# Kernel tuning notes

Hardware: AMD Instinct MI355X
Metric: run time of the kernel (lower is better)

The kernel has to match this reference:

```python
import jax, jax.numpy as jnp
import numpy as np

N = 50000   # nodes
E = 800000  # edges
C = 64      # channels per head (= n_channel)
H = 2       # heads
EPS = 1e-5


def _layernorm(x, g, b):
    m = jnp.mean(x, axis=-1, keepdims=True)
    v = jnp.mean((x - m) ** 2, axis=-1, keepdims=True)
    return (x - m) / jnp.sqrt(v + EPS) * g + b


def setup_inputs() -> dict:
    key = jax.random.key(0)
    ks = jax.random.split(key, 20)
    r = lambda k, shape: (jax.random.normal(k, shape, jnp.float32) * 0.05)
    inp = {
        "x": jax.random.normal(ks[0], (N, C), jnp.float32),
        "edge_index": jax.random.randint(ks[1], (2, E), 0, N, jnp.int64),
        "edge_attr": jax.random.normal(ks[2], (E, 1), jnp.float32),
        # TransformerConv params (PyG): lin_query/key/value: in=C -> H*C with bias
        "Wq": r(ks[3], (H * C, C)), "bq": r(ks[4], (H * C,)),
        "Wk": r(ks[5], (H * C, C)), "bk": r(ks[6], (H * C,)),
        "Wv": r(ks[7], (H * C, C)), "bv": r(ks[8], (H * C,)),
        # lin_edge: edge_dim=1 -> H*C, no bias
        "We": r(ks[9], (H * C, 1)),
        # lin_skip (root weight, concat=False -> out=C), with bias
        "Wskip": r(ks[10], (C, C)), "bskip": r(ks[11], (C,)),
        # shell linear + layernorms
        "Wl": r(ks[12], (C, C)), "bl": r(ks[13], (C,)),
        "g0": jnp.ones((C,), jnp.float32), "b0": jnp.zeros((C,), jnp.float32),
        "g1": jnp.ones((C,), jnp.float32), "b1": jnp.zeros((C,), jnp.float32),
    }
    return inp


def _transformer_conv(x, src, dst, edge_attr, Wq, bq, Wk, bk, Wv, bv, We, Wskip, bskip):
    q = (x @ Wq.T + bq).reshape(N, H, C)
    k = (x @ Wk.T + bk).reshape(N, H, C)
    v = (x @ Wv.T + bv).reshape(N, H, C)
    e = (edge_attr @ We.T).reshape(E, H, C)        # [E,H,C]
    k_j = k[src] + e                               # gather + edge key
    v_j = v[src] + e
    alpha = jnp.einsum('ehc,ehc->eh', q[dst], k_j) / jnp.sqrt(jnp.float32(C))
    # segment softmax over destination nodes
    amax = jax.ops.segment_max(alpha, dst, num_segments=N)      # [N,H]
    ex = jnp.exp(alpha - amax[dst])
    denom = jax.ops.segment_sum(ex, dst, num_segments=N)        # [N,H]
    w = ex / denom[dst]                                          # [E,H]
    out = jax.ops.segment_sum(v_j * w[..., None], dst, num_segments=N)  # [N,H,C]
    out = out.mean(axis=1)                                       # concat=False -> mean heads
    return out + x @ Wskip.T + bskip                             # root weight skip


def reference(x, edge_index, edge_attr, Wq, bq, Wk, bk, Wv, bv, We, Wskip, bskip,
              Wl, bl, g0, b0, g1, b1):
    src, dst = edge_index[0], edge_index[1]
    h = _transformer_conv(x, src, dst, edge_attr, Wq, bq, Wk, bk, Wv, bv, We, Wskip, bskip)
    x = x + _layernorm(h, g0, b0)
    x = x + _layernorm(x @ Wl.T + bl, g1, b1)
    return x
```

## Files before the change

kernel.cpp:

```cpp
#include <hip/hip_runtime.h>
#include <hip/hip_fp16.h>

#define NN 50000
#define NE 800000

typedef unsigned short u16;
typedef float v2f __attribute__((ext_vector_type(2)));

template <int CTRL>
__device__ __forceinline__ float dpp_add(float p) {
  const int v = __builtin_amdgcn_update_dpp(0, __float_as_int(p), CTRL, 0xF, 0xF, true);
  return p + __int_as_float(v);
}
__device__ __forceinline__ float red16(float p) {
  p = dpp_add<0xB1>(p);
  p = dpp_add<0x4E>(p);
  p = dpp_add<0x141>(p);
  p = dpp_add<0x140>(p);
  return p;
}

__global__ __launch_bounds__(256) void k_gemm_qkv(
    const float* __restrict__ x,
    const float* __restrict__ Wq, const float* __restrict__ bq,
    const float* __restrict__ Wk, const float* __restrict__ bk,
    const float* __restrict__ Wv, const float* __restrict__ bv,
    const float* __restrict__ Wskip, const float* __restrict__ bskip,
    const int* __restrict__ ei, int* __restrict__ cnt, int* __restrict__ pos,
    float* __restrict__ qs, unsigned* __restrict__ kvp, float* __restrict__ skip)
{
  const int t = threadIdx.x;
  const int y = blockIdx.y;

  if (y == 2) {
    const int e0 = blockIdx.x * 1024 + t;
    #pragma unroll
    for (int it = 0; it < 4; it++) {
      const int e = e0 + it * 256;
      if (e < NE) pos[e] = atomicAdd(&cnt[ei[NE + e]], 1);
    }
    return;
  }

  __shared__ float xsT[64][68];
  __shared__ float wsT[64][68];
  const int tileN = blockIdx.x * 64;

  {
    const int nl = t >> 2, c0 = (t & 3) * 16;
    const int n = tileN + nl;
    float4 a0, a1, a2, a3;
    if (n < NN) {
      const float4* xr = (const float4*)(x + (size_t)n * 64 + c0);
      a0 = xr[0]; a1 = xr[1]; a2 = xr[2]; a3 = xr[3];
    } else {
      a0 = a1 = a2 = a3 = make_float4(0.f, 0.f, 0.f, 0.f);
    }
    xsT[c0 +  0][nl] = a0.x; xsT[c0 +  1][nl] = a0.y; xsT[c0 +  2][nl] = a0.z; xsT[c0 +  3][nl] = a0.w;
    xsT[c0 +  4][nl] = a1.x; xsT[c0 +  5][nl] = a1.y; xsT[c0 +  6][nl] = a1.z; xsT[c0 +  7][nl] = a1.w;
    xsT[c0 +  8][nl] = a2.x; xsT[c0 +  9][nl] = a2.y; xsT[c0 + 10][nl] = a2.z; xsT[c0 + 11][nl] = a2.w;
    xsT[c0 + 12][nl] = a3.x; xsT[c0 + 13][nl] = a3.y; xsT[c0 + 14][nl] = a3.z; xsT[c0 + 15][nl] = a3.w;
  }

  const int tx = t & 15, ty = t >> 4;
  const int nslices = (y == 0) ? 3 : 4;

  for (int s = 0; s < nslices; s++) {
    const int jt = (y == 0) ? ((s == 2) ? 6 : s) : (s + 2);
    const float* W; const float* bias; int rowbase;
    if (jt < 2)      { W = Wq;    bias = bq;    rowbase = jt * 64; }
    else if (jt < 4) { W = Wk;    bias = bk;    rowbase = (jt - 2) * 64; }
    else if (jt < 6) { W = Wv;    bias = bv;    rowbase = (jt - 4) * 64; }
    else             { W = Wskip; bias = bskip; rowbase = 0; }

    __syncthreads();
    {
      const int nl = t >> 2, c0 = (t & 3) * 16;
      const float4* wr = (const float4*)(W + (size_t)(rowbase + nl) * 64 + c0);
      float4 b0 = wr[0], b1 = wr[1], b2 = wr[2], b3 = wr[3];
      wsT[c0 +  0][nl] = b0.x; wsT[c0 +  1][nl] = b0.y; wsT[c0 +  2][nl] = b0.z; wsT[c0 +  3][nl] = b0.w;
      wsT[c0 +  4][nl] = b1.x; wsT[c0 +  5][nl] = b1.y; wsT[c0 +  6][nl] = b1.z; wsT[c0 +  7][nl] = b1.w;
      wsT[c0 +  8][nl] = b2.x; wsT[c0 +  9][nl] = b2.y; wsT[c0 + 10][nl] = b2.z; wsT[c0 + 11][nl] = b2.w;
      wsT[c0 + 12][nl] = b3.x; wsT[c0 + 13][nl] = b3.y; wsT[c0 + 14][nl] = b3.z; wsT[c0 + 15][nl] = b3.w;
    }
    __syncthreads();

    float acc[4][4];
    #pragma unroll
    for (int i = 0; i < 4; i++)
      #pragma unroll
      for (int j = 0; j < 4; j++) acc[i][j] = 0.f;

    #pragma unroll 8
    for (int kk = 0; kk < 64; kk++) {
      float4 a = *(const float4*)&xsT[kk][tx * 4];
      float4 b = *(const float4*)&wsT[kk][ty * 4];
      acc[0][0] += a.x * b.x; acc[0][1] += a.x * b.y; acc[0][2] += a.x * b.z; acc[0][3] += a.x * b.w;
      acc[1][0] += a.y * b.x; acc[1][1] += a.y * b.y; acc[1][2] += a.y * b.z; acc[1][3] += a.y * b.w;
      acc[2][0] += a.z * b.x; acc[2][1] += a.z * b.y; acc[2][2] += a.z * b.z; acc[2][3] += a.z * b.w;
      acc[3][0] += a.w * b.x; acc[3][1] += a.w * b.y; acc[3][2] += a.w * b.z; acc[3][3] += a.w * b.w;
    }

    const int n0 = tileN + tx * 4;
    const int col0 = rowbase + ty * 4;
    const float4 bb = *(const float4*)(bias + col0);
    #pragma unroll
    for (int i = 0; i < 4; i++) {
      const int n = n0 + i;
      if (n >= NN) continue;
      const float r0 = acc[i][0] + bb.x, r1 = acc[i][1] + bb.y;
      const float r2 = acc[i][2] + bb.z, r3 = acc[i][3] + bb.w;
      if (jt < 2) {
        *(float4*)(qs + (size_t)n * 128 + col0) = make_float4(r0, r1, r2, r3);
      } else if (jt < 6) {
        const int entry = col0 >> 2;
        unsigned pk = 0;
        pk = __builtin_amdgcn_cvt_pk_fp8_f32(r0, r1, pk, false);
        pk = __builtin_amdgcn_cvt_pk_fp8_f32(r2, r3, pk, true);
        kvp[(size_t)n * 64 + entry * 2 + ((jt >= 4) ? 1 : 0)] = pk;
      } else {
        *(float4*)(skip + (size_t)n * 64 + col0) = make_float4(r0, r1, r2, r3);
      }
    }
  }
}

__global__ __launch_bounds__(1024) void k_scan(
    const int* __restrict__ cnt, int* __restrict__ rowptr) {
  __shared__ int wsum[16];
  __shared__ int boff_s;
  const int t = threadIdx.x, lane = t & 63, wid = t >> 6;
  const int b = blockIdx.x;

  {
    int pre = 0;
    for (int j = t; j < b * 1024; j += 1024) pre += cnt[j];
    #pragma unroll
    for (int m = 1; m <= 32; m <<= 1) pre += __shfl_xor(pre, m);
    if (lane == 0) wsum[wid] = pre;
    __syncthreads();
    if (t == 0) {
      int s = 0;
      #pragma unroll
      for (int j = 0; j < 16; j++) s += wsum[j];
      boff_s = s;
    }
    __syncthreads();
  }

  const int i = b * 1024 + t;
  const int val = (i < NN) ? cnt[i] : 0;
  int incl = val;
  #pragma unroll
  for (int off = 1; off < 64; off <<= 1) {
    int n = __shfl_up(incl, off, 64);
    if (lane >= off) incl += n;
  }
  if (lane == 63) wsum[wid] = incl;
  __syncthreads();
  if (t < 16) {
    int wv = wsum[t];
    int wincl = wv;
    #pragma unroll
    for (int off = 1; off < 16; off <<= 1) {
      int n = __shfl_up(wincl, off, 64);
      if (t >= off) wincl += n;
    }
    wsum[t] = wincl - wv;
  }
  __syncthreads();
  if (i < NN) rowptr[i] = boff_s + wsum[wid] + incl - val;
  if (b == 0 && t == 0) rowptr[NN] = NE;
}

__global__ __launch_bounds__(256) void k_fill(
    const int* __restrict__ ei, const float* __restrict__ ea,
    const int* __restrict__ rowptr, const int* __restrict__ pos,
    unsigned* __restrict__ epk) {
  const int e = blockIdx.x * 256 + threadIdx.x;
  if (e < NE) {
    const int dst = ei[NE + e];
    const int idx = rowptr[dst] + pos[e];
    const unsigned rec = (unsigned)ei[e] |
        ((unsigned)__half_as_ushort(__float2half_rn(ea[e])) << 16);
    epk[idx] = rec;
  }
}

__global__ __launch_bounds__(256) void k_fused(
    const float* __restrict__ qs, const unsigned* __restrict__ kvp,
    const float* __restrict__ skip, const float* __restrict__ x,
    const int* __restrict__ rowptr, const unsigned* __restrict__ epk,
    const float* __restrict__ We,
    const float* __restrict__ Wl, const float* __restrict__ bl,
    const float* __restrict__ g0, const float* __restrict__ b0,
    const float* __restrict__ g1, const float* __restrict__ b1,
    float* __restrict__ out)
{
  __shared__ float wlT[64][65];
  __shared__ float scx[4][64];
  const int t = threadIdx.x;
  {
    const int jl = t >> 2, c0 = (t & 3) * 16;
    const float4* wr = (const float4*)(Wl + (size_t)jl * 64 + c0);
    float4 w0 = wr[0], w1 = wr[1], w2 = wr[2], w3 = wr[3];
    wlT[c0 +  0][jl] = w0.x; wlT[c0 +  1][jl] = w0.y; wlT[c0 +  2][jl] = w0.z; wlT[c0 +  3][jl] = w0.w;
    wlT[c0 +  4][jl] = w1.x; wlT[c0 +  5][jl] = w1.y; wlT[c0 +  6][jl] = w1.z; wlT[c0 +  7][jl] = w1.w;
    wlT[c0 +  8][jl] = w2.x; wlT[c0 +  9][jl] = w2.y; wlT[c0 + 10][jl] = w2.z; wlT[c0 + 11][jl] = w2.w;
    wlT[c0 + 12][jl] = w3.x; wlT[c0 + 13][jl] = w3.y; wlT[c0 + 14][jl] = w3.z; wlT[c0 + 15][jl] = w3.w;
  }
  __syncthreads();

  const int w = t >> 6;
  const int dst = __builtin_amdgcn_readfirstlane(blockIdx.x * 4 + w);
  const int lane = t & 63;
  const int half = lane >> 5;
  const int el = lane & 31;

  const float4 qv = ((const float4*)(qs + (size_t)dst * 128))[el];
  const float4 we4 = ((const float4*)We)[el];
  const float skipv = skip[(size_t)dst * 64 + lane];
  const float xv    = x[(size_t)dst * 64 + lane];

  const float qwe = red16(qv.x * we4.x + qv.y * we4.y + qv.z * we4.z + qv.w * we4.w);

  const int base = rowptr[dst];
  const int deg  = rowptr[dst + 1] - base;
  const uint2* kv8 = (const uint2*)kvp;
  const unsigned* ep = epk + base;

  float s = 0.f, sw = 0.f;
  float sv0 = 0.f, sv1 = 0.f, sv2 = 0.f, sv3 = 0.f;

  const float SCL = 0.18033688011112042f;

#define UNPACK_W(er) __half2float(__ushort_as_half((unsigned short)((er) >> 16)))
#define PROC(u, wg, mask)                                                   \
  {                                                                         \
    const v2f k01 = __builtin_amdgcn_cvt_pk_f32_fp8((u).x, false);          \
    const v2f k23 = __builtin_amdgcn_cvt_pk_f32_fp8((u).x, true);           \
    const v2f v01 = __builtin_amdgcn_cvt_pk_f32_fp8((u).y, false);          \
    const v2f v23 = __builtin_amdgcn_cvt_pk_f32_fp8((u).y, true);           \
    const float p = red16(qv.x * k01.x + qv.y * k01.y +                     \
                          qv.z * k23.x + qv.w * k23.y);                     \
    float e_ = exp2f((p + (wg) * qwe) * SCL);                               \
    e_ = (mask) ? e_ : 0.f;                                                 \
    s += e_; sw += e_ * (wg);                                               \
    sv0 += e_ * v01.x; sv1 += e_ * v01.y;                                   \
    sv2 += e_ * v23.x; sv3 += e_ * v23.y;                                   \
  }

  int i = 0;
  for (; i + 8 <= deg; i += 8) {
    const unsigned er0 = ep[i + half];
    const unsigned er1 = ep[i + 2 + half];
    const unsigned er2 = ep[i + 4 + half];
    const unsigned er3 = ep[i + 6 + half];
    const uint2 u0 = kv8[(size_t)(er0 & 0xFFFFu) * 32 + el];
    const uint2 u1 = kv8[(size_t)(er1 & 0xFFFFu) * 32 + el];
    const uint2 u2 = kv8[(size_t)(er2 & 0xFFFFu) * 32 + el];
    const uint2 u3 = kv8[(size_t)(er3 & 0xFFFFu) * 32 + el];
    PROC(u0, UNPACK_W(er0), true)
    PROC(u1, UNPACK_W(er1), true)
    PROC(u2, UNPACK_W(er2), true)
    PROC(u3, UNPACK_W(er3), true)
  }
  for (; i + 4 <= deg; i += 4) {
    const unsigned er0 = ep[i + half];
    const unsigned er1 = ep[i + 2 + half];
    const uint2 u0 = kv8[(size_t)(er0 & 0xFFFFu) * 32 + el];
    const uint2 u1 = kv8[(size_t)(er1 & 0xFFFFu) * 32 + el];
    PROC(u0, UNPACK_W(er0), true)
    PROC(u1, UNPACK_W(er1), true)
  }
  for (; i < deg; i += 2) {
    const int idx = i + half;
    const bool valid = idx < deg;
    const unsigned er = ep[valid ? idx : (deg - 1)];
    const uint2 u = kv8[(size_t)(er & 0xFFFFu) * 32 + el];
    PROC(u, UNPACK_W(er), valid)
  }
#undef PROC
#undef UNPACK_W

  s  += __shfl_xor(s, 32);
  sw += __shfl_xor(sw, 32);
  sv0 += __shfl_xor(sv0, 32); sv1 += __shfl_xor(sv1, 32);
  sv2 += __shfl_xor(sv2, 32); sv3 += __shfl_xor(sv3, 32);

  float a0 = 0.f, a1 = 0.f, a2 = 0.f, a3 = 0.f;
  if (deg > 0) {
    const float inv = 1.f / s;
    a0 = (sv0 + sw * we4.x) * inv;
    a1 = (sv1 + sw * we4.y) * inv;
    a2 = (sv2 + sw * we4.z) * inv;
    a3 = (sv3 + sw * we4.w) * inv;
  }
  a0 = 0.5f * (a0 + __shfl_xor(a0, 16));
  a1 = 0.5f * (a1 + __shfl_xor(a1, 16));
  a2 = 0.5f * (a2 + __shfl_xor(a2, 16));
  a3 = 0.5f * (a3 + __shfl_xor(a3, 16));
  if (half == 0 && el < 16) {
    ((float4*)scx[w])[el] = make_float4(a0, a1, a2, a3);
  }
  const float hv = scx[w][lane] + skipv;

  float m1 = hv, m2 = hv * hv;
  m1 = red16(m1); m2 = red16(m2);
  m1 += __shfl_xor(m1, 16); m2 += __shfl_xor(m2, 16);
  m1 += __shfl_xor(m1, 32); m2 += __shfl_xor(m2, 32);
  const float mean = m1 * (1.f / 64.f);
  const float var = fmaxf(m2 * (1.f / 64.f) - mean * mean, 0.f);
  const float x1 = xv + (hv - mean) * rsqrtf(var + 1e-5f) * g0[lane] + b0[lane];

  scx[w][lane] = x1;
  float y0 = 0.f, y1 = 0.f, y2 = 0.f, y3 = 0.f;
  #pragma unroll
  for (int kk = 0; kk < 64; kk += 4) {
    const float4 xb = *(const float4*)&scx[w][kk];
    y0 += xb.x * wlT[kk][lane];
    y1 += xb.y * wlT[kk + 1][lane];
    y2 += xb.z * wlT[kk + 2][lane];
    y3 += xb.w * wlT[kk + 3][lane];
  }
  const float y = bl[lane] + (y0 + y1) + (y2 + y3);

  float n1 = y, n2 = y * y;
  n1 = red16(n1); n2 = red16(n2);
  n1 += __shfl_xor(n1, 16); n2 += __shfl_xor(n2, 16);
  n1 += __shfl_xor(n1, 32); n2 += __shfl_xor(n2, 32);
  const float mean2 = n1 * (1.f / 64.f);
  const float var2 = fmaxf(n2 * (1.f / 64.f) - mean2 * mean2, 0.f);
  out[(size_t)dst * 64 + lane] = x1 + (y - mean2) * rsqrtf(var2 + 1e-5f) * g1[lane] + b1[lane];
}

extern "C" void kernel_launch(void* const* d_in, const int* in_sizes, int n_in,
                              void* d_out, int out_size, void* d_ws, size_t ws_size,
                              hipStream_t stream) {
  const float* x     = (const float*)d_in[0];
  const int*   ei    = (const int*)d_in[1];
  const float* ea    = (const float*)d_in[2];
  const float* Wq    = (const float*)d_in[3];
  const float* bq    = (const float*)d_in[4];
  const float* Wk    = (const float*)d_in[5];
  const float* bk    = (const float*)d_in[6];
  const float* Wv    = (const float*)d_in[7];
  const float* bv    = (const float*)d_in[8];
  const float* We    = (const float*)d_in[9];
  const float* Wskip = (const float*)d_in[10];
  const float* bskip = (const float*)d_in[11];
  const float* Wl    = (const float*)d_in[12];
  const float* bl    = (const float*)d_in[13];
  const float* g0    = (const float*)d_in[14];
  const float* b0    = (const float*)d_in[15];
  const float* g1    = (const float*)d_in[16];
  const float* b1    = (const float*)d_in[17];
  float* out = (float*)d_out;

  float* ws = (float*)d_ws;
  size_t off = 0;
  float* qs   = ws + off; off += (size_t)NN * 128;
  unsigned* kvp = (unsigned*)(ws + off); off += (size_t)NN * 64;
  float* skip = ws + off; off += (size_t)NN * 64;
  int* cnt    = (int*)(ws + off); off += NN;
  int* rowptr = (int*)(ws + off); off += NN + 1;
  int* pos    = (int*)(ws + off); off += NE;
  unsigned* epk = (unsigned*)(ws + off); off += NE;

  (void)hipMemsetAsync(cnt, 0, (size_t)NN * sizeof(int), stream);

  dim3 gGemm((NN + 63) / 64, 3);
  hipLaunchKernelGGL(k_gemm_qkv, gGemm, dim3(256), 0, stream,
                     x, Wq, bq, Wk, bk, Wv, bv, Wskip, bskip, ei, cnt, pos, qs, kvp, skip);
  hipLaunchKernelGGL(k_scan, dim3(49), dim3(1024), 0, stream, cnt, rowptr);
  hipLaunchKernelGGL(k_fill, dim3((NE + 255) / 256), dim3(256), 0, stream,
                     ei, ea, rowptr, pos, epk);
  hipLaunchKernelGGL(k_fused, dim3(NN / 4), dim3(256), 0, stream,
                     qs, kvp, skip, x, rowptr, epk, We,
                     Wl, bl, g0, b0, g1, b1, out);
}
```

Measured before the change: 150.7 us.

## Use bf16 MFMA for QKV/skip projection GEMM in a single block row

Replaces the scalar fp32 outer-product GEMM with bf16 MFMA 16x16x32 instructions, converting x and weight tiles to bf16 in shared memory. Each block now computes all seven 64-column slices (Q, K, V, skip) instead of splitting them across two grid rows, so the x tile is loaded once per node tile. K/V results are staged through a shared buffer and then packed to fp8. This adds bf16 rounding to the projection inputs and a few extra shared-memory round trips, but cuts the FMA instruction count of the GEMM stage.

```diff
diff --git a/kernel.cpp b/kernel.cpp
--- a/kernel.cpp
+++ b/kernel.cpp
@@ -6,6 +6,8 @@
 
 typedef unsigned short u16;
 typedef float v2f __attribute__((ext_vector_type(2)));
+typedef short bf16x8 __attribute__((ext_vector_type(8)));
+typedef float f32x4 __attribute__((ext_vector_type(4)));
 
 template <int CTRL>
 __device__ __forceinline__ float dpp_add(float p) {
@@ -18,6 +20,14 @@
   p = dpp_add<0x141>(p);
   p = dpp_add<0x140>(p);
   return p;
+}
+
+__device__ __forceinline__ unsigned short f2bf(float f) {
+  unsigned u = __float_as_uint(f);
+  return (unsigned short)((u + 0x7FFFu + ((u >> 16) & 1u)) >> 16);
+}
+__device__ __forceinline__ unsigned pk2(float a, float b) {
+  return (unsigned)f2bf(a) | ((unsigned)f2bf(b) << 16);
 }
 
 __global__ __launch_bounds__(256) void k_gemm_qkv(
@@ -30,9 +40,8 @@
     float* __restrict__ qs, unsigned* __restrict__ kvp, float* __restrict__ skip)
 {
   const int t = threadIdx.x;
-  const int y = blockIdx.y;
-
-  if (y == 2) {
+
+  if (blockIdx.y == 1) {
     const int e0 = blockIdx.x * 1024 + t;
     #pragma unroll
     for (int it = 0; it < 4; it++) {
@@ -42,8 +51,9 @@
     return;
   }
 
-  __shared__ float xsT[64][68];
-  __shared__ float wsT[64][68];
+  __shared__ unsigned short xb[64][72];
+  __shared__ unsigned short wb[64][72];
+  __shared__ float cb[64][68];
   const int tileN = blockIdx.x * 64;
 
   {
@@ -56,70 +66,92 @@
     } else {
       a0 = a1 = a2 = a3 = make_float4(0.f, 0.f, 0.f, 0.f);
     }
-    xsT[c0 +  0][nl] = a0.x; xsT[c0 +  1][nl] = a0.y; xsT[c0 +  2][nl] = a0.z; xsT[c0 +  3][nl] = a0.w;
-    xsT[c0 +  4][nl] = a1.x; xsT[c0 +  5][nl] = a1.y; xsT[c0 +  6][nl] = a1.z; xsT[c0 +  7][nl] = a1.w;
-    xsT[c0 +  8][nl] = a2.x; xsT[c0 +  9][nl] = a2.y; xsT[c0 + 10][nl] = a2.z; xsT[c0 + 11][nl] = a2.w;
-    xsT[c0 + 12][nl] = a3.x; xsT[c0 + 13][nl] = a3.y; xsT[c0 + 14][nl] = a3.z; xsT[c0 + 15][nl] = a3.w;
-  }
-
-  const int tx = t & 15, ty = t >> 4;
-  const int nslices = (y == 0) ? 3 : 4;
-
-  for (int s = 0; s < nslices; s++) {
-    const int jt = (y == 0) ? ((s == 2) ? 6 : s) : (s + 2);
-    const float* W; const float* bias; int rowbase;
-    if (jt < 2)      { W = Wq;    bias = bq;    rowbase = jt * 64; }
-    else if (jt < 4) { W = Wk;    bias = bk;    rowbase = (jt - 2) * 64; }
-    else if (jt < 6) { W = Wv;    bias = bv;    rowbase = (jt - 4) * 64; }
-    else             { W = Wskip; bias = bskip; rowbase = 0; }
+    *(uint4*)&xb[nl][c0] =
+        make_uint4(pk2(a0.x, a0.y), pk2(a0.z, a0.w), pk2(a1.x, a1.y), pk2(a1.z, a1.w));
+    *(uint4*)&xb[nl][c0 + 8] =
+        make_uint4(pk2(a2.x, a2.y), pk2(a2.z, a2.w), pk2(a3.x, a3.y), pk2(a3.z, a3.w));
+  }
+
+  const int w = t >> 6;
+  const int l = t & 63;
+  const int rb = w * 16;
+  const int frow = l & 15;
+  const int fk = (l >> 4) * 8;
+
+  const bf16x8 a0 = *(const bf16x8*)&xb[rb + frow][fk];
+  const bf16x8 a1 = *(const bf16x8*)&xb[rb + frow][fk + 32];
+
+  for (int s = 0; s < 7; s++) {
+    const float* Wb; const float* bias; int cbase; int kind;
+    switch (s) {
+      case 0: Wb = Wq;    bias = bq;    cbase = 0;  kind = 0; break;
+      case 1: Wb = Wq;    bias = bq;    cbase = 64; kind = 0; break;
+      case 2: Wb = Wk;    bias = bk;    cbase = 0;  kind = 2; break;
+      case 3: Wb = Wv;    bias = bv;    cbase = 0;  kind = 3; break;
+      case 4: Wb = Wk;    bias = bk;    cbase = 64; kind = 2; break;
+      case 5: Wb = Wv;    bias = bv;    cbase = 64; kind = 3; break;
+      default: Wb = Wskip; bias = bskip; cbase = 0; kind = 1; break;
+    }
 
     __syncthreads();
     {
       const int nl = t >> 2, c0 = (t & 3) * 16;
-      const float4* wr = (const float4*)(W + (size_t)(rowbase + nl) * 64 + c0);
+      const float4* wr = (const float4*)(Wb + (size_t)(cbase + nl) * 64 + c0);
       float4 b0 = wr[0], b1 = wr[1], b2 = wr[2], b3 = wr[3];
-      wsT[c0 +  0][nl] = b0.x; wsT[c0 +  1][nl] = b0.y; wsT[c0 +  2][nl] = b0.z; wsT[c0 +  3][nl] = b0.w;
-      wsT[c0 +  4][nl] = b1.x; wsT[c0 +  5][nl] = b1.y; wsT[c0 +  6][nl] = b1.z; wsT[c0 +  7][nl] = b1.w;
-      wsT[c0 +  8][nl] = b2.x; wsT[c0 +  9][nl] = b2.y; wsT[c0 + 10][nl] = b2.z; wsT[c0 + 11][nl] = b2.w;
-      wsT[c0 + 12][nl] = b3.x; wsT[c0 + 13][nl] = b3.y; wsT[c0 + 14][nl] = b3.z; wsT[c0 + 15][nl] = b3.w;
+      *(uint4*)&wb[nl][c0] =
+          make_uint4(pk2(b0.x, b0.y), pk2(b0.z, b0.w), pk2(b1.x, b1.y), pk2(b1.z, b1.w));
+      *(uint4*)&wb[nl][c0 + 8] =
+          make_uint4(pk2(b2.x, b2.y), pk2(b2.z, b2.w), pk2(b3.x, b3.y), pk2(b3.z, b3.w));
     }
     __syncthreads();
 
-    float acc[4][4];
     #pragma unroll
-    for (int i = 0; i < 4; i++)
-      #pragma unroll
-      for (int j = 0; j < 4; j++) acc[i][j] = 0.f;
-
-    #pragma unroll 8
-    for (int kk = 0; kk < 64; kk++) {
-      float4 a = *(const float4*)&xsT[kk][tx * 4];
-      float4 b = *(const float4*)&wsT[kk][ty * 4];
-      acc[0][0] += a.x * b.x; acc[0][1] += a.x * b.y; acc[0][2] += a.x * b.z; acc[0][3] += a.x * b.w;
-      acc[1][0] += a.y * b.x; acc[1][1] += a.y * b.y; acc[1][2] += a.y * b.z; acc[1][3] += a.y * b.w;
-      acc[2][0] += a.z * b.x; acc[2][1] += a.z * b.y; acc[2][2] += a.z * b.z; acc[2][3] += a.z * b.w;
-      acc[3][0] += a.w * b.x; acc[3][1] += a.w * b.y; acc[3][2] += a.w * b.z; acc[3][3] += a.w * b.w;
-    }
-
-    const int n0 = tileN + tx * 4;
-    const int col0 = rowbase + ty * 4;
-    const float4 bb = *(const float4*)(bias + col0);
-    #pragma unroll
-    for (int i = 0; i < 4; i++) {
-      const int n = n0 + i;
-      if (n >= NN) continue;
-      const float r0 = acc[i][0] + bb.x, r1 = acc[i][1] + bb.y;
-      const float r2 = acc[i][2] + bb.z, r3 = acc[i][3] + bb.w;
-      if (jt < 2) {
-        *(float4*)(qs + (size_t)n * 128 + col0) = make_float4(r0, r1, r2, r3);
-      } else if (jt < 6) {
-        const int entry = col0 >> 2;
-        unsigned pk = 0;
-        pk = __builtin_amdgcn_cvt_pk_fp8_f32(r0, r1, pk, false);
-        pk = __builtin_amdgcn_cvt_pk_fp8_f32(r2, r3, pk, true);
-        kvp[(size_t)n * 64 + entry * 2 + ((jt >= 4) ? 1 : 0)] = pk;
+    for (int ct = 0; ct < 4; ct++) {
+      const bf16x8 b0 = *(const bf16x8*)&wb[ct * 16 + frow][fk];
+      const bf16x8 b1 = *(const bf16x8*)&wb[ct * 16 + frow][fk + 32];
+      f32x4 acc = {0.f, 0.f, 0.f, 0.f};
+      acc = __builtin_amdgcn_mfma_f32_16x16x32_bf16(a0, b0, acc, 0, 0, 0);
+      acc = __builtin_amdgcn_mfma_f32_16x16x32_bf16(a1, b1, acc, 0, 0, 0);
+      const int col = ct * 16 + frow;
+      const int row0 = rb + ((l >> 4) << 2);
+      const float bb = bias[cbase * (kind != 1 ? 1 : 0) + col];
+      if (kind == 0) {
+        #pragma unroll
+        for (int j = 0; j < 4; j++) {
+          const int n = tileN + row0 + j;
+          if (n < NN) qs[(size_t)n * 128 + cbase + col] = acc[j] + bb;
+        }
+      } else if (kind == 1) {
+        #pragma unroll
+        for (int j = 0; j < 4; j++) {
+          const int n = tileN + row0 + j;
+          if (n < NN) skip[(size_t)n * 64 + col] = acc[j] + bb;
+        }
       } else {
-        *(float4*)(skip + (size_t)n * 64 + col0) = make_float4(r0, r1, r2, r3);
+        #pragma unroll
+        for (int j = 0; j < 4; j++) cb[row0 + j][col] = acc[j] + bb;
+      }
+    }
+
+    if (kind >= 2) {
+      const int rrow = rb + (l >> 2);
+      const int chb = (l & 3) * 16;
+      const int n = tileN + rrow;
+      if (n < NN) {
+        const float4* c4 = (const float4*)&cb[rrow][chb];
+        const float4 c0_ = c4[0], c1_ = c4[1], c2_ = c4[2], c3_ = c4[3];
+        unsigned p0 = 0, p1 = 0, p2 = 0, p3 = 0;
+        p0 = __builtin_amdgcn_cvt_pk_fp8_f32(c0_.x, c0_.y, p0, false);
+        p0 = __builtin_amdgcn_cvt_pk_fp8_f32(c0_.z, c0_.w, p0, true);
+        p1 = __builtin_amdgcn_cvt_pk_fp8_f32(c1_.x, c1_.y, p1, false);
+        p1 = __builtin_amdgcn_cvt_pk_fp8_f32(c1_.z, c1_.w, p1, true);
+        p2 = __builtin_amdgcn_cvt_pk_fp8_f32(c2_.x, c2_.y, p2, false);
+        p2 = __builtin_amdgcn_cvt_pk_fp8_f32(c2_.z, c2_.w, p2, true);
+        p3 = __builtin_amdgcn_cvt_pk_fp8_f32(c3_.x, c3_.y, p3, false);
+        p3 = __builtin_amdgcn_cvt_pk_fp8_f32(c3_.z, c3_.w, p3, true);
+        const int ebase = (cbase + chb) >> 2;
+        unsigned* dstp = kvp + (size_t)n * 64 + ebase * 2 + ((kind == 3) ? 1 : 0);
+        dstp[0] = p0; dstp[2] = p1; dstp[4] = p2; dstp[6] = p3;
       }
     }
   }
@@ -317,11 +349,11 @@
   float y0 = 0.f, y1 = 0.f, y2 = 0.f, y3 = 0.f;
   #pragma unroll
   for (int kk = 0; kk < 64; kk += 4) {
-    const float4 xb = *(const float4*)&scx[w][kk];
-    y0 += xb.x * wlT[kk][lane];
-    y1 += xb.y * wlT[kk + 1][lane];
-    y2 += xb.z * wlT[kk + 2][lane];
-    y3 += xb.w * wlT[kk + 3][lane];
+    const float4 xb4 = *(const float4*)&scx[w][kk];
+    y0 += xb4.x * wlT[kk][lane];
+    y1 += xb4.y * wlT[kk + 1][lane];
+    y2 += xb4.z * wlT[kk + 2][lane];
+    y3 += xb4.w * wlT[kk + 3][lane];
   }
   const float y = bl[lane] + (y0 + y1) + (y2 + y3);
 
@@ -369,7 +401,7 @@
 
   (void)hipMemsetAsync(cnt, 0, (size_t)NN * sizeof(int), stream);
 
-  dim3 gGemm((NN + 63) / 64, 3);
+  dim3 gGemm((NN + 63) / 64, 2);
   hipLaunchKernelGGL(k_gemm_qkv, gGemm, dim3(256), 0, stream,
                      x, Wq, bq, Wk, bk, Wv, bv, Wskip, bskip, ei, cnt, pos, qs, kvp, skip);
   hipLaunchKernelGGL(k_scan, dim3(49), dim3(1024), 0, stream, cnt, rowptr);
```

After: 141.2 us (median of 2 runs). 1.07x faster.
